# Performance work log

Measured on AMD Instinct MI355X. Metric: run time of the kernel, lower is better.

Reference implementation:

```python
import jax, jax.numpy as jnp
import numpy as np

N = 100000   # nodes
E = 1600000  # edges
D = 128      # feature dim
DO = 3       # out_head target dim
C = 50000    # centers


def setup_inputs() -> dict:
    key = jax.random.key(0)
    k1, k2, k3, k4 = jax.random.split(key, 4)
    H = jax.random.normal(k1, (N, D), dtype=jnp.float32)
    W = jax.random.normal(k2, (D, DO), dtype=jnp.float32) / np.sqrt(D)
    b = jnp.zeros((DO,), dtype=jnp.float32)
    target = jax.random.normal(k3, (N, DO), dtype=jnp.float32)
    edge_index = jax.random.randint(k4, (2, E), 0, N, dtype=jnp.int32)
    centers = jnp.arange(C, dtype=jnp.int32)  # distinct center node ids
    return {"H": H, "W": W, "b": b, "target": target,
            "edge_index": edge_index, "centers": centers}


def reference(H, W, b, target, edge_index, centers):
    # Vectorized equivalent of the per-center Python loop:
    # for each edge (s, d): if s is a center, pair (owner(s), d) contributes
    # mean-squared error of out_head(H[d]) vs target[d]; then per-center mean,
    # then mean over all centers (empty centers contribute 0 via cnt clamp).
    n_nodes = H.shape[0]
    n_centers = centers.shape[0]
    # node id -> center slot (n_centers == "not a center" sentinel)
    owner_of = jnp.full((n_nodes,), n_centers, dtype=jnp.int32)
    owner_of = owner_of.at[centers].set(jnp.arange(n_centers, dtype=jnp.int32))
    src, dst = edge_index[0], edge_index[1]
    owners = owner_of[src]              # [E]
    mask = owners < n_centers           # [E] edge rooted at a center

    z_frontier = H[dst]                 # [E, D] neighbor-feature gather
    y_hat = z_frontier @ W + b          # [E, DO] out_head (linear)
    y_true = target[dst]                # [E, DO]
    err = jnp.mean((y_hat - y_true) ** 2, axis=-1)  # [E]
    errm = jnp.where(mask, err, jnp.zeros((), err.dtype))

    # segment-mean per center; sentinel bucket n_centers dropped
    loss_sum = jax.ops.segment_sum(errm, owners, num_segments=n_centers + 1)[:n_centers]
    cnt = jax.ops.segment_sum(mask.astype(err.dtype), owners,
                              num_segments=n_centers + 1)[:n_centers]
    aux_loss = jnp.mean(loss_sum / jnp.maximum(cnt, 1.0))
    return aux_loss
```

## Files before the change

### kernel.cpp

```cpp
#include <hip/hip_runtime.h>


#define CNT_SHIFT 44
#define ERR_SCALE 67108864.0f
#define BKT_SHIFT 8
#define BKT_SIZE  256
#define P2B       256
#define BKT_THR   1024
#define ERRBLKS   2048
#define STASH     6272
#define PREF_STRIDE 200

__device__ __forceinline__ int owner_fn(int s, bool fast, int C,
                                        const int* __restrict__ arr_idx,
                                        const int* __restrict__ centers) {
    if (fast) return (s < C) ? s : -1;
    int i = arr_idx[s];
    return ((unsigned)i < (unsigned)C && centers[i] == s) ? i : -1;
}

__global__ __launch_bounds__(256)
void prep_err_kernel(const float* __restrict__ H, const float* __restrict__ W,
                     const float* __restrict__ b, const float* __restrict__ target,
                     const int* __restrict__ centers,
                     float* __restrict__ err_node,
                     int* __restrict__ arr_idx,
                     int* __restrict__ flagpart,
                     float* __restrict__ out,
                     int N, int C, int NBV, int out_size) {
    __shared__ int ok;
    const int t = threadIdx.x;
    const int gtid = blockIdx.x * 256 + t;

    if (blockIdx.x < NBV) {
        if (t == 0) ok = 1;
        __syncthreads();
        bool mism = false;
        if (gtid < C) {
            int c = centers[gtid];
            arr_idx[c] = gtid;
            mism = (c != gtid);
        }
        if (__ballot(mism) != 0ull && (t & 63) == 0) atomicAnd(&ok, 0);
        __syncthreads();
        if (t == 0) flagpart[blockIdx.x] = ok;
    }
    if (gtid >= 1 && gtid < out_size) out[gtid] = 0.f;

    const int lane = t & 63, sub = lane >> 5, l32 = lane & 31;
    float wr[12];
    {
        const float* wb = W + (size_t)(4 * l32) * 3;
        #pragma unroll
        for (int r = 0; r < 12; ++r) wr[r] = wb[r];
    }
    const float b0 = b[0], b1 = b[1], b2 = b[2];
    const float4* H4 = reinterpret_cast<const float4*>(H);
    const int wv    = blockIdx.x * 4 + (t >> 6);
    const int EW    = ERRBLKS * 4;
    const int npair = (N + 1) >> 1;
    for (int p = wv; p < npair; p += EW) {
        const int node = 2 * p + sub;
        float4 hv = (node < N) ? H4[(size_t)node * 32 + l32]
                               : make_float4(0.f, 0.f, 0.f, 0.f);
        float hx[4] = {hv.x, hv.y, hv.z, hv.w};
        float a0 = 0.f, a1 = 0.f, a2 = 0.f;
        #pragma unroll
        for (int r = 0; r < 4; ++r) {
            a0 += hx[r] * wr[r * 3 + 0];
            a1 += hx[r] * wr[r * 3 + 1];
            a2 += hx[r] * wr[r * 3 + 2];
        }
        #pragma unroll
        for (int m = 16; m > 0; m >>= 1) {
            a0 += __shfl_xor(a0, m, 64);
            a1 += __shfl_xor(a1, m, 64);
            a2 += __shfl_xor(a2, m, 64);
        }
        if (l32 == 0 && node < N) {
            float e0 = a0 + b0 - target[(size_t)node * 3 + 0];
            float e1 = a1 + b1 - target[(size_t)node * 3 + 1];
            float e2 = a2 + b2 - target[(size_t)node * 3 + 2];
            err_node[node] = (e0*e0 + e1*e1 + e2*e2) * (1.0f / 3.0f);
        }
    }
}

__global__ __launch_bounds__(BKT_THR)
void bucketize_kernel(const int* __restrict__ eidx,
                      const int* __restrict__ centers,
                      const int* __restrict__ arr_idx,
                      const int* __restrict__ flagpart,
                      unsigned short* __restrict__ pref_g,
                      unsigned int* __restrict__ pairs,
                      int E, int C, int NB, int NBV) {
    __shared__ unsigned int stash[STASH];
    __shared__ unsigned int hist[256];
    __shared__ unsigned int scan[256];
    __shared__ unsigned int total_sh;
    __shared__ int okf;
    const int t = threadIdx.x;

    if (t == 0) okf = 1;
    if (t < 256) hist[t] = 0u;
    __syncthreads();
    bool my_ok = (t < NBV) ? (flagpart[t] != 0) : true;
    if (__ballot(!my_ok) != 0ull && (t & 63) == 0) atomicAnd(&okf, 0);
    __syncthreads();
    const bool fast = (okf != 0);

    const int E4     = E >> 2;
    const int chunk4 = (E4 + P2B - 1) / P2B;
    const int c0     = blockIdx.x * chunk4;
    const int c1     = min(E4, c0 + chunk4);
    const int4* r0 = reinterpret_cast<const int4*>(eidx);
    const int4* r1 = reinterpret_cast<const int4*>(eidx + E);

    for (int i = c0 + t; i < c1; i += BKT_THR) {
        int4 s4 = r0[i];
        int ss[4] = {s4.x, s4.y, s4.z, s4.w};
        #pragma unroll
        for (int k = 0; k < 4; ++k) {
            int o = owner_fn(ss[k], fast, C, arr_idx, centers);
            if (o >= 0) atomicAdd(&hist[(unsigned)o >> BKT_SHIFT], 1u);
        }
    }
    __syncthreads();
    if (t < 256) scan[t] = hist[t];
    __syncthreads();
    for (int off = 1; off < 256; off <<= 1) {
        unsigned v = (t < 256 && t >= off) ? scan[t - off] : 0u;
        __syncthreads();
        if (t < 256 && t >= off) scan[t] += v;
        __syncthreads();
    }
    if (t < 256) {
        unsigned pre = (t == 0) ? 0u : scan[t - 1];
        hist[t] = pre;
        if (t <= NB)
            pref_g[(size_t)blockIdx.x * PREF_STRIDE + t] = (unsigned short)pre;
    }
    if (t == 0) total_sh = scan[255];
    __syncthreads();
    for (int i = c0 + t; i < c1; i += BKT_THR) {
        int4 s4 = r0[i];
        int4 d4 = r1[i];
        int ss[4] = {s4.x, s4.y, s4.z, s4.w};
        int dd[4] = {d4.x, d4.y, d4.z, d4.w};
        #pragma unroll
        for (int k = 0; k < 4; ++k) {
            int o = owner_fn(ss[k], fast, C, arr_idx, centers);
            if (o >= 0) {
                unsigned bk = (unsigned)o >> BKT_SHIFT;
                unsigned pos = atomicAdd(&hist[bk], 1u);
                stash[pos] = (((unsigned)o & (BKT_SIZE - 1)) << 17)
                           | (unsigned)dd[k];
            }
        }
    }
    __syncthreads();
    {
        unsigned nvec = (total_sh + 3u) >> 2;
        uint4*       dg = reinterpret_cast<uint4*>(pairs + (size_t)blockIdx.x * STASH);
        const uint4* sg = reinterpret_cast<const uint4*>(stash);
        for (unsigned i = t; i < nvec; i += BKT_THR) dg[i] = sg[i];
    }
}

__global__ __launch_bounds__(1024)
void reduce_kernel(const unsigned int* __restrict__ pairs,
                   const unsigned short* __restrict__ pref_g,
                   const float* __restrict__ err_node,
                   float* __restrict__ partial, int C) {
    __shared__ unsigned long long bins[BKT_SIZE];
    __shared__ float wsum[16];
    const int bk = blockIdx.x, t = threadIdx.x;
    if (t < BKT_SIZE) bins[t] = 0ull;
    __syncthreads();
    {
        const int seg = t >> 2;
        const int j   = t & 3;
        const size_t pb = (size_t)seg * PREF_STRIDE;
        unsigned start = pref_g[pb + bk];
        unsigned end   = pref_g[pb + bk + 1];
        const unsigned int* reg = pairs + (size_t)seg * STASH;
        for (unsigned i = start + j; i < end; i += 4) {
            unsigned p = reg[i];
            float err = err_node[p & 0x1FFFFu];
            atomicAdd(&bins[p >> 17],
                      (1ull << CNT_SHIFT) + (unsigned long long)(err * ERR_SCALE));
        }
    }
    __syncthreads();
    float term = 0.f;
    if (t < BKT_SIZE) {
        int center = bk * BKT_SIZE + t;
        if (center < C) {
            unsigned long long u = bins[t];
            float cnt = (float)(u >> CNT_SHIFT);
            float es  = (float)(u & ((1ull << CNT_SHIFT) - 1)) * (1.0f / ERR_SCALE);
            term = es / fmaxf(cnt, 1.0f);
        }
    }
    #pragma unroll
    for (int m = 32; m > 0; m >>= 1) term += __shfl_down(term, m, 64);
    if ((t & 63) == 0) wsum[t >> 6] = term;
    __syncthreads();
    if (t == 0) {
        float s = 0.f;
        #pragma unroll
        for (int w = 0; w < 16; ++w) s += wsum[w];
        partial[bk] = s;
    }
}

__global__ __launch_bounds__(256)
void final_kernel(const float* __restrict__ partial,
                  float* __restrict__ out, int NB, float invC) {
    __shared__ float wsum[4];
    const int t = threadIdx.x;
    float v = (t < NB) ? partial[t] : 0.f;
    #pragma unroll
    for (int m = 32; m > 0; m >>= 1) v += __shfl_down(v, m, 64);
    if ((t & 63) == 0) wsum[t >> 6] = v;
    __syncthreads();
    if (t == 0) out[0] = (wsum[0] + wsum[1] + wsum[2] + wsum[3]) * invC;
}

__global__ __launch_bounds__(256)
void fb_err_kernel(const float* __restrict__ H, const float* __restrict__ W,
                   const float* __restrict__ b, const float* __restrict__ target,
                   const int* __restrict__ centers,
                   float* __restrict__ err_node, int* __restrict__ arr_idx,
                   float* __restrict__ out, int N, int C, int D, int DO,
                   int out_size) {
    int gtid = blockIdx.x * blockDim.x + threadIdx.x;
    if (gtid < C) arr_idx[centers[gtid]] = gtid;
    if (gtid < out_size) out[gtid] = 0.f;
    if (gtid < N) {
        float acc = 0.f;
        for (int j = 0; j < DO; ++j) {
            float a = b[j];
            for (int r = 0; r < D; ++r)
                a += H[(size_t)gtid * D + r] * W[(size_t)r * DO + j];
            float e = a - target[(size_t)gtid * DO + j];
            acc += e * e;
        }
        err_node[gtid] = acc / (float)DO;
    }
}

__global__ void fb_edge_kernel(const int* __restrict__ eidx,
                               const int* __restrict__ arr_idx,
                               const int* __restrict__ centers,
                               const float* __restrict__ err_node,
                               unsigned long long* __restrict__ binsg,
                               int E, int C) {
    int e = blockIdx.x * blockDim.x + threadIdx.x;
    if (e >= E) return;
    int s = eidx[e];
    int o = owner_fn(s, false, C, arr_idx, centers);
    if (o >= 0) {
        int d = eidx[E + e];
        unsigned long long add = (1ull << CNT_SHIFT)
                               + (unsigned long long)(err_node[d] * ERR_SCALE);
        atomicAdd(&binsg[o], add);
    }
}

__global__ void fb_finalize_kernel(const unsigned long long* __restrict__ binsg,
                                   float* __restrict__ out, int C) {
    int i = blockIdx.x * blockDim.x + threadIdx.x;
    float term = 0.f;
    if (i < C) {
        unsigned long long u = binsg[i];
        float cnt = (float)(u >> CNT_SHIFT);
        float es  = (float)(u & ((1ull << CNT_SHIFT) - 1)) * (1.0f / ERR_SCALE);
        term = es / fmaxf(cnt, 1.0f);
    }
    #pragma unroll
    for (int m = 32; m > 0; m >>= 1) term += __shfl_down(term, m, 64);
    __shared__ float wsum[4];
    if ((threadIdx.x & 63) == 0) wsum[threadIdx.x >> 6] = term;
    __syncthreads();
    if (threadIdx.x == 0)
        atomicAdd(out, (wsum[0] + wsum[1] + wsum[2] + wsum[3]) / (float)C);
}

extern "C" void kernel_launch(void* const* d_in, const int* in_sizes, int n_in,
                              void* d_out, int out_size, void* d_ws, size_t ws_size,
                              hipStream_t stream) {
    const float* H      = (const float*)d_in[0];
    const float* W      = (const float*)d_in[1];
    const float* b      = (const float*)d_in[2];
    const float* target = (const float*)d_in[3];
    const int*   eidx   = (const int*)d_in[4];
    const int*   ctrs   = (const int*)d_in[5];

    const int DO = in_sizes[2];
    const int D  = in_sizes[1] / DO;
    const int N  = in_sizes[0] / D;
    const int E  = in_sizes[4] / 2;
    const int C  = in_sizes[5];
    const int NB  = (C + BKT_SIZE - 1) >> BKT_SHIFT;
    const int NBV = (C + 255) / 256;

    size_t off = 0;
    auto take = [&](size_t bytes) {
        void* p = (char*)d_ws + off;
        off = (off + bytes + 255) & ~255ull;
        return p;
    };
    float*          err_node = (float*)take((size_t)N * 4);
    int*            arr_idx  = (int*)take((size_t)N * 4);
    int*            flagpart = (int*)take((size_t)NBV * 4);
    unsigned short* pref_g   = (unsigned short*)take((size_t)P2B * PREF_STRIDE * 2);
    float*          partial  = (float*)take((size_t)NB * 4);
    unsigned int*   pairs    = (unsigned int*)((char*)d_ws + off);
    size_t need = off + (size_t)P2B * STASH * 4;

    int chunk_edges = 4 * ((E / 4 + P2B - 1) / P2B);
    bool fits = (ws_size >= need) && (NB + 1 <= PREF_STRIDE) && (NBV <= BKT_THR) &&
                (NBV <= ERRBLKS) && (N < (1 << 17)) && ((E & 3) == 0) &&
                (chunk_edges <= STASH) && (D == 128) && (DO == 3) && (out_size >= 1);
    if (fits) {
        prep_err_kernel<<<ERRBLKS, 256, 0, stream>>>(H, W, b, target, ctrs,
                                                     err_node, arr_idx, flagpart,
                                                     (float*)d_out, N, C, NBV,
                                                     out_size);
        bucketize_kernel<<<P2B, BKT_THR, 0, stream>>>(eidx, ctrs, arr_idx,
                                                      flagpart, pref_g, pairs,
                                                      E, C, NB, NBV);
        reduce_kernel<<<NB, 1024, 0, stream>>>(pairs, pref_g, err_node,
                                               partial, C);
        final_kernel<<<1, 256, 0, stream>>>(partial, (float*)d_out, NB,
                                            1.0f / (float)C);
    } else {
        unsigned long long* binsg = (unsigned long long*)((char*)d_ws + off);
        hipMemsetAsync(binsg, 0, (size_t)C * 8, stream);
        int thr = 256;
        fb_err_kernel<<<(max(N, C) + thr - 1) / thr, thr, 0, stream>>>(
            H, W, b, target, ctrs, err_node, arr_idx, (float*)d_out,
            N, C, D, DO, out_size);
        fb_edge_kernel<<<(E + thr - 1) / thr, thr, 0, stream>>>(
            eidx, arr_idx, ctrs, err_node, binsg, E, C);
        fb_finalize_kernel<<<(C + thr - 1) / thr, thr, 0, stream>>>(
            binsg, (float*)d_out, C);
    }
}
```

Measured before the change: 34.87 us.

## Use per-thread node error, cache sources in LDS, fold final reduce into atomics

The node error computation becomes one thread per node, with double-buffered float4 loads of the feature row replacing half-wave shuffle reductions. The bucketize kernel stashes source ids in shared memory so the second pass does not reload them from global memory. The final reduction kernel is removed; each reduce block atomically adds its scaled partial into the output. This saves a launch and redundant global reads, but the per-thread row reads are less coalesced and the extra LDS may lower occupancy.

```diff
diff --git a/kernel.cpp b/kernel.cpp
--- a/kernel.cpp
+++ b/kernel.cpp
@@ -7,7 +7,6 @@
 #define BKT_SIZE  256
 #define P2B       256
 #define BKT_THR   1024
-#define ERRBLKS   2048
 #define STASH     6272
 #define PREF_STRIDE 200
 
@@ -45,45 +44,42 @@
         __syncthreads();
         if (t == 0) flagpart[blockIdx.x] = ok;
     }
-    if (gtid >= 1 && gtid < out_size) out[gtid] = 0.f;
-
-    const int lane = t & 63, sub = lane >> 5, l32 = lane & 31;
-    float wr[12];
-    {
-        const float* wb = W + (size_t)(4 * l32) * 3;
-        #pragma unroll
-        for (int r = 0; r < 12; ++r) wr[r] = wb[r];
-    }
-    const float b0 = b[0], b1 = b[1], b2 = b[2];
-    const float4* H4 = reinterpret_cast<const float4*>(H);
-    const int wv    = blockIdx.x * 4 + (t >> 6);
-    const int EW    = ERRBLKS * 4;
-    const int npair = (N + 1) >> 1;
-    for (int p = wv; p < npair; p += EW) {
-        const int node = 2 * p + sub;
-        float4 hv = (node < N) ? H4[(size_t)node * 32 + l32]
-                               : make_float4(0.f, 0.f, 0.f, 0.f);
-        float hx[4] = {hv.x, hv.y, hv.z, hv.w};
-        float a0 = 0.f, a1 = 0.f, a2 = 0.f;
-        #pragma unroll
-        for (int r = 0; r < 4; ++r) {
-            a0 += hx[r] * wr[r * 3 + 0];
-            a1 += hx[r] * wr[r * 3 + 1];
-            a2 += hx[r] * wr[r * 3 + 2];
-        }
-        #pragma unroll
-        for (int m = 16; m > 0; m >>= 1) {
-            a0 += __shfl_xor(a0, m, 64);
-            a1 += __shfl_xor(a1, m, 64);
-            a2 += __shfl_xor(a2, m, 64);
-        }
-        if (l32 == 0 && node < N) {
-            float e0 = a0 + b0 - target[(size_t)node * 3 + 0];
-            float e1 = a1 + b1 - target[(size_t)node * 3 + 1];
-            float e2 = a2 + b2 - target[(size_t)node * 3 + 2];
-            err_node[node] = (e0*e0 + e1*e1 + e2*e2) * (1.0f / 3.0f);
-        }
-    }
+    if (gtid < out_size) out[gtid] = 0.f;
+
+    const int node = gtid;
+    if (node >= N) return;
+    const float4* Hr = reinterpret_cast<const float4*>(H) + (size_t)node * 32;
+
+    float a0 = 0.f, a1 = 0.f, a2 = 0.f;
+    float4 ra[8], rb[8];
+
+    #define LOADG(arr, g)                                                   \
+        { _Pragma("unroll")                                                 \
+          for (int i = 0; i < 8; ++i) arr[i] = Hr[(g) * 8 + i]; }
+    #define COMPG(arr, g)                                                   \
+        { _Pragma("unroll")                                                 \
+          for (int i = 0; i < 8; ++i) {                                     \
+              float hx[4] = {arr[i].x, arr[i].y, arr[i].z, arr[i].w};       \
+              _Pragma("unroll")                                             \
+              for (int e = 0; e < 4; ++e) {                                 \
+                  const int k = (g) * 32 + i * 4 + e;                       \
+                  a0 += hx[e] * W[k * 3 + 0];                               \
+                  a1 += hx[e] * W[k * 3 + 1];                               \
+                  a2 += hx[e] * W[k * 3 + 2];                               \
+              }                                                             \
+          } }
+
+    LOADG(ra, 0) LOADG(rb, 1)
+    COMPG(ra, 0) LOADG(ra, 2)
+    COMPG(rb, 1) LOADG(rb, 3)
+    COMPG(ra, 2) COMPG(rb, 3)
+    #undef LOADG
+    #undef COMPG
+
+    float e0 = a0 + b[0] - target[(size_t)node * 3 + 0];
+    float e1 = a1 + b[1] - target[(size_t)node * 3 + 1];
+    float e2 = a2 + b[2] - target[(size_t)node * 3 + 2];
+    err_node[node] = (e0 * e0 + e1 * e1 + e2 * e2) * (1.0f / 3.0f);
 }
 
 __global__ __launch_bounds__(BKT_THR)
@@ -95,6 +91,7 @@
                       unsigned int* __restrict__ pairs,
                       int E, int C, int NB, int NBV) {
     __shared__ unsigned int stash[STASH];
+    __shared__ int          src_c[STASH];
     __shared__ unsigned int hist[256];
     __shared__ unsigned int scan[256];
     __shared__ unsigned int total_sh;
@@ -118,6 +115,7 @@
 
     for (int i = c0 + t; i < c1; i += BKT_THR) {
         int4 s4 = r0[i];
+        reinterpret_cast<int4*>(src_c)[i - c0] = s4;
         int ss[4] = {s4.x, s4.y, s4.z, s4.w};
         #pragma unroll
         for (int k = 0; k < 4; ++k) {
@@ -143,8 +141,8 @@
     if (t == 0) total_sh = scan[255];
     __syncthreads();
     for (int i = c0 + t; i < c1; i += BKT_THR) {
-        int4 s4 = r0[i];
         int4 d4 = r1[i];
+        int4 s4 = reinterpret_cast<const int4*>(src_c)[i - c0];
         int ss[4] = {s4.x, s4.y, s4.z, s4.w};
         int dd[4] = {d4.x, d4.y, d4.z, d4.w};
         #pragma unroll
@@ -171,7 +169,7 @@
 void reduce_kernel(const unsigned int* __restrict__ pairs,
                    const unsigned short* __restrict__ pref_g,
                    const float* __restrict__ err_node,
-                   float* __restrict__ partial, int C) {
+                   float* __restrict__ out, int C, float invC) {
     __shared__ unsigned long long bins[BKT_SIZE];
     __shared__ float wsum[16];
     const int bk = blockIdx.x, t = threadIdx.x;
@@ -210,21 +208,8 @@
         float s = 0.f;
         #pragma unroll
         for (int w = 0; w < 16; ++w) s += wsum[w];
-        partial[bk] = s;
-    }
-}
-
-__global__ __launch_bounds__(256)
-void final_kernel(const float* __restrict__ partial,
-                  float* __restrict__ out, int NB, float invC) {
-    __shared__ float wsum[4];
-    const int t = threadIdx.x;
-    float v = (t < NB) ? partial[t] : 0.f;
-    #pragma unroll
-    for (int m = 32; m > 0; m >>= 1) v += __shfl_down(v, m, 64);
-    if ((t & 63) == 0) wsum[t >> 6] = v;
-    __syncthreads();
-    if (t == 0) out[0] = (wsum[0] + wsum[1] + wsum[2] + wsum[3]) * invC;
+        atomicAdd(out, s * invC);
+    }
 }
 
 __global__ __launch_bounds__(256)
@@ -304,6 +289,7 @@
     const int C  = in_sizes[5];
     const int NB  = (C + BKT_SIZE - 1) >> BKT_SHIFT;
     const int NBV = (C + 255) / 256;
+    const int EB  = (N + 255) / 256;
 
     size_t off = 0;
     auto take = [&](size_t bytes) {
@@ -315,26 +301,23 @@
     int*            arr_idx  = (int*)take((size_t)N * 4);
     int*            flagpart = (int*)take((size_t)NBV * 4);
     unsigned short* pref_g   = (unsigned short*)take((size_t)P2B * PREF_STRIDE * 2);
-    float*          partial  = (float*)take((size_t)NB * 4);
     unsigned int*   pairs    = (unsigned int*)((char*)d_ws + off);
     size_t need = off + (size_t)P2B * STASH * 4;
 
     int chunk_edges = 4 * ((E / 4 + P2B - 1) / P2B);
     bool fits = (ws_size >= need) && (NB + 1 <= PREF_STRIDE) && (NBV <= BKT_THR) &&
-                (NBV <= ERRBLKS) && (N < (1 << 17)) && ((E & 3) == 0) &&
+                (NBV <= EB) && (N < (1 << 17)) && ((E & 3) == 0) &&
                 (chunk_edges <= STASH) && (D == 128) && (DO == 3) && (out_size >= 1);
     if (fits) {
-        prep_err_kernel<<<ERRBLKS, 256, 0, stream>>>(H, W, b, target, ctrs,
-                                                     err_node, arr_idx, flagpart,
-                                                     (float*)d_out, N, C, NBV,
-                                                     out_size);
+        prep_err_kernel<<<EB, 256, 0, stream>>>(H, W, b, target, ctrs,
+                                                err_node, arr_idx, flagpart,
+                                                (float*)d_out, N, C, NBV,
+                                                out_size);
         bucketize_kernel<<<P2B, BKT_THR, 0, stream>>>(eidx, ctrs, arr_idx,
                                                       flagpart, pref_g, pairs,
                                                       E, C, NB, NBV);
         reduce_kernel<<<NB, 1024, 0, stream>>>(pairs, pref_g, err_node,
-                                               partial, C);
-        final_kernel<<<1, 256, 0, stream>>>(partial, (float*)d_out, NB,
-                                            1.0f / (float)C);
+                                               (float*)d_out, C, 1.0f / (float)C);
     } else {
         unsigned long long* binsg = (unsigned long long*)((char*)d_ws + off);
         hipMemsetAsync(binsg, 0, (size_t)C * 8, stream);
```

Result: no change. 34.24 us (-1.8%).
